# Optimization experiments

Measured on AMD Instinct MI355X. Metric: run time of the kernel, lower is better.

The kernel has to match this reference:

```python
import jax, jax.numpy as jnp
import numpy as np

# Config (matches init_kwargs)
L, B, D, V = 12, 8, 2048, 32000
H, HD, G, N, K = 64, 64, 8, 128, 4
I = H * HD                 # intermediate_size = 4096
CONV = I + 2 * G * N       # conv_dim = 6144
P = I + CONV + H           # in_proj output = 10304
TMAX = 10000.0             # finite replacement for inf time_step_limit


def rmsnorm(x, w, eps=1e-5):
    x32 = x.astype(jnp.float32)
    return (x32 * jax.lax.rsqrt(jnp.mean(x32 * x32, axis=-1, keepdims=True) + eps)) * w


def setup_inputs() -> dict:
    key = jax.random.key(0)
    ks = jax.random.split(key, 10)
    s = 0.02
    return {
        "input_ids": jax.random.randint(ks[0], (B, 1), 0, V),
        "conv_states": jax.random.normal(ks[1], (L, B, CONV, K), dtype=jnp.float32),
        "ssm_states": jax.random.normal(ks[2], (L, B, H, HD, N), dtype=jnp.float32) * 0.1,
        "emb": jax.random.normal(ks[3], (V, D), dtype=jnp.float32) * s,
        "norm_w": jnp.ones((L, D), jnp.float32),
        "in_proj_w": jax.random.normal(ks[4], (L, D, P), dtype=jnp.float32) * s,
        "conv_w": jax.random.normal(ks[5], (L, CONV, K), dtype=jnp.float32) * s,
        "conv_b": jnp.zeros((L, CONV), jnp.float32),
        "dt_bias": jax.random.normal(ks[6], (L, H), dtype=jnp.float32) * s,
        "A_log": jnp.log(jnp.broadcast_to(jnp.arange(1, H + 1, dtype=jnp.float32), (L, H))),
        "D_param": jnp.ones((L, H), jnp.float32),
        "gn_w": jnp.ones((L, I), jnp.float32),
        "out_proj_w": jax.random.normal(ks[7], (L, I, D), dtype=jnp.float32) * s,
        "norm_f_w": jnp.ones((D,), jnp.float32),
        "lm_head_w": jax.random.normal(ks[8], (V, D), dtype=jnp.float32) * s,
    }


def reference(input_ids, conv_states, ssm_states, emb, norm_w, in_proj_w, conv_w,
              conv_b, dt_bias, A_log, D_param, gn_w, out_proj_w, norm_f_w, lm_head_w):
    h = emb[input_ids]  # [B,1,D]

    def layer(h, xs):
        cs, ss, nw, wi, cw, cb, db, al, dp, gw, wo = xs
        residual = h
        hn = rmsnorm(h, nw)                                   # block.norm (RMSNorm)
        proj = jnp.einsum('btd,dp->btp', hn, wi)              # in_proj
        gate, hBC, dt = jnp.split(proj, [I, I + CONV], axis=-1)
        # conv state shift + depthwise conv over kernel dim
        new_in = hBC[:, 0, :]                                 # [B, CONV]
        new_cs = jnp.concatenate([cs[:, :, 1:], new_in[:, :, None]], axis=-1)  # [B,CONV,K]
        conv_out = jnp.sum(new_cs * cw[None], axis=-1) + cb
        conv_out = jax.nn.silu(conv_out)
        x, Bv, Cv = jnp.split(conv_out, [I, I + G * N], axis=-1)
        x = x.reshape(B, H, HD)
        # dt: softplus(dt + dt_bias), clamp to [0, 10000]
        dt_ = jax.nn.softplus(dt[:, 0, :] + db[None, :])       # [B,H]
        dt_ = jnp.clip(dt_, 0.0, TMAX)
        A = -jnp.exp(al)                                       # [H], fp32
        dA = jnp.exp(dt_[:, :, None, None] * A[None, :, None, None])  # [B,H,1,1]
        rep = H // G
        Brep = jnp.repeat(Bv.reshape(B, G, N), rep, axis=1)    # [B,H,N]
        Crep = jnp.repeat(Cv.reshape(B, G, N), rep, axis=1)
        dBx = dt_[:, :, None, None] * Brep[:, :, None, :] * x[:, :, :, None]  # [B,H,HD,N]
        new_ss = ss * dA + dBx
        y = jnp.sum(new_ss * Crep[:, :, None, :], axis=-1)     # [B,H,HD]
        y = y + x * dp[None, :, None]                          # skip via D
        y = y.reshape(B, 1, I)
        # gated RMSNorm: (y * silu(gate)) -> rmsnorm * weight
        yg = y.astype(jnp.float32) * jax.nn.silu(gate.astype(jnp.float32))
        y = rmsnorm(yg, gw)
        out = jnp.einsum('bti,id->btd', y, wo)                 # out_proj
        return residual + out, (new_cs, new_ss)

    h, (new_conv, new_ssm) = jax.lax.scan(
        layer, h,
        (conv_states, ssm_states, norm_w, in_proj_w, conv_w, conv_b,
         dt_bias, A_log, D_param, gn_w, out_proj_w))
    hf = rmsnorm(h, norm_f_w)                                  # norm_f
    logits = jnp.einsum('btd,vd->btv', hf, lm_head_w).astype(jnp.float32)
    return logits, new_conv, new_ssm
```

## Files before the change

kernel.cpp:

```cpp
#include <hip/hip_runtime.h>
#include <hip/hip_bf16.h>
#include <math.h>

#define LNUM 12
#define BNUM 8
#define DNUM 2048
#define VNUM 32000
#define HNUM 64
#define HDNUM 64
#define GNUM 8
#define NNUM 128
#define KNUM 4
#define INUM (HNUM*HDNUM)
#define CONVNUM (INUM + 2*GNUM*NNUM)
#define PNUM (INUM + CONVNUM + HNUM)

#define IP_KC 16
#define OP_KC 64

__device__ __forceinline__ float sigmoidf_(float x){ return 1.f/(1.f+expf(-x)); }

__global__ void k_embed(const int* __restrict__ ids, const float* __restrict__ emb,
                        float* __restrict__ h, float* __restrict__ sqp){
  int b = blockIdx.x; int t = threadIdx.x;
  const float* src = emb + (size_t)ids[b]*DNUM;
  float* dst = h + (size_t)b*DNUM;
  for (int d = t*4; d < DNUM; d += 256*4)
    *(float4*)(dst + d) = *(const float4*)(src + d);
  __shared__ float red[4];
  for (int j = 0; j < 8; ++j){
    float v = src[j*256 + t];
    float q = v*v;
    q += __shfl_xor(q,32); q += __shfl_xor(q,16); q += __shfl_xor(q,8);
    q += __shfl_xor(q,4);  q += __shfl_xor(q,2);  q += __shfl_xor(q,1);
    if ((t & 63) == 0) red[t>>6] = q;
    __syncthreads();
    if (t == 0) sqp[b*8 + j] = red[0]+red[1]+red[2]+red[3];
    __syncthreads();
  }
}

__global__ __launch_bounds__(256) void k_inproj(const float* __restrict__ h,
                                                const float* __restrict__ sqp,
                                                const float* __restrict__ nw,
                                                const float* __restrict__ W,
                                                float* __restrict__ part1){
  int t = threadIdx.x, w = t >> 6, l = t & 63;
  int pb = blockIdx.x, kc = blockIdx.y;
  __shared__ float xs[BNUM][128];
  __shared__ float invs[BNUM];
  __shared__ float4 red[4][BNUM][64];
  if (t < 64){
    int b = t>>3, j = t&7;
    float v = sqp[b*8 + j];
    v += __shfl_xor(v,1); v += __shfl_xor(v,2); v += __shfl_xor(v,4);
    if (j == 0) invs[b] = rsqrtf(v*(1.f/DNUM) + 1e-5f);
  }
  __syncthreads();
  int r0 = kc*128;
  for (int i = t; i < BNUM*128; i += 256){
    int b = i>>7, dl = i&127;
    xs[b][dl] = h[b*DNUM + r0 + dl] * invs[b] * nw[r0 + dl];
  }
  __syncthreads();
  int p0 = pb*256 + l*4;
  bool valid = (p0 < PNUM);
  float4 acc[BNUM];
  #pragma unroll
  for (int b = 0; b < BNUM; ++b) acc[b] = make_float4(0.f,0.f,0.f,0.f);
  if (valid){
    int rbase = w*32;
    const float* wp = W + (size_t)(r0 + rbase)*PNUM + p0;
    #pragma unroll 4
    for (int r = 0; r < 32; ++r){
      float4 w4 = *(const float4*)wp;
      wp += PNUM;
      #pragma unroll
      for (int b = 0; b < BNUM; ++b){
        float xv = xs[b][rbase + r];
        acc[b].x += xv*w4.x; acc[b].y += xv*w4.y; acc[b].z += xv*w4.z; acc[b].w += xv*w4.w;
      }
    }
  }
  #pragma unroll
  for (int b = 0; b < BNUM; ++b) red[w][b][l] = acc[b];
  __syncthreads();
  if (w == 0 && valid){
    #pragma unroll
    for (int b = 0; b < BNUM; ++b){
      float4 s0 = red[0][b][l], s1 = red[1][b][l], s2 = red[2][b][l], s3 = red[3][b][l];
      float4 s;
      s.x = (s0.x+s1.x)+(s2.x+s3.x);
      s.y = (s0.y+s1.y)+(s2.y+s3.y);
      s.z = (s0.z+s1.z)+(s2.z+s3.z);
      s.w = (s0.w+s1.w)+(s2.w+s3.w);
      *(float4*)(part1 + (size_t)(kc*BNUM + b)*PNUM + p0) = s;
    }
  }
}

__global__ void k_convfuse(const float* __restrict__ part1,
                           const float* __restrict__ cs_in, float* __restrict__ cs_out,
                           const float* __restrict__ cw, const float* __restrict__ cb,
                           const float* __restrict__ db, const float* __restrict__ al,
                           float* __restrict__ projg, float* __restrict__ convout,
                           float* __restrict__ dtv, float* __restrict__ dAv){
  int idx = blockIdx.x*256 + threadIdx.x;
  int b = idx / PNUM, p = idx - b*PNUM;
  float v = 0.f;
  #pragma unroll
  for (int kc = 0; kc < IP_KC; ++kc) v += part1[(size_t)(kc*BNUM + b)*PNUM + p];
  if (p < INUM){
    projg[b*INUM + p] = v;
  } else if (p < INUM + CONVNUM){
    int c = p - INUM;
    int sid = b*CONVNUM + c;
    float4 s = *(const float4*)(cs_in + (size_t)sid*KNUM);
    float4 ns = make_float4(s.y, s.z, s.w, v);
    *(float4*)(cs_out + (size_t)sid*KNUM) = ns;
    float4 w = *(const float4*)(cw + c*KNUM);
    float co = ns.x*w.x + ns.y*w.y + ns.z*w.z + ns.w*w.w + cb[c];
    convout[b*CONVNUM + c] = co * sigmoidf_(co);
  } else {
    int hh = p - INUM - CONVNUM;
    float dtr = v + db[hh];
    float dt = (dtr > 20.f) ? dtr : log1pf(expf(dtr));
    dt = fminf(fmaxf(dt, 0.f), 10000.f);
    float A = -expf(al[hh]);
    dtv[b*HNUM + hh] = dt;
    dAv[b*HNUM + hh] = expf(dt*A);
  }
}

__global__ __launch_bounds__(256) void k_ssm(const float* __restrict__ ss_in,
                                             const float* __restrict__ convout,
                                             const float* __restrict__ projg,
                                             const float* __restrict__ dtv,
                                             const float* __restrict__ dAv,
                                             const float* __restrict__ D_param,
                                             float* __restrict__ ss_out,
                                             float* __restrict__ yg,
                                             float* __restrict__ ygsq){
  int b = blockIdx.x >> 6, hh = blockIdx.x & 63;
  int t = threadIdx.x;
  __shared__ float Bs[NNUM], Cs[NNUM];
  __shared__ float sred[8];
  int g = hh >> 3;
  if (t < NNUM) Bs[t] = convout[b*CONVNUM + INUM + g*NNUM + t];
  else          Cs[t-NNUM] = convout[b*CONVNUM + INUM + GNUM*NNUM + g*NNUM + (t-NNUM)];
  __syncthreads();
  float dt = dtv[b*HNUM + hh];
  float dA = dAv[b*HNUM + hh];
  float dp = D_param[hh];
  int r = t & 31, a = t >> 5;
  float4 Bv = *(float4*)&Bs[r*4];
  float4 Cv = *(float4*)&Cs[r*4];
  const float* sin_ = ss_in  + (size_t)(b*HNUM + hh)*HDNUM*NNUM;
  float*       sout = ss_out + (size_t)(b*HNUM + hh)*HDNUM*NNUM;
  float s_yg = 0.f;
  #pragma unroll
  for (int k = 0; k < 8; ++k){
    int hd = k*8 + a;
    float xv = convout[b*CONVNUM + hh*HDNUM + hd];
    float coef = dt * xv;
    int off = k*1024 + t*4;
    float4 s4 = *(const float4*)(sin_ + off);
    float4 ns;
    ns.x = s4.x*dA + coef*Bv.x;
    ns.y = s4.y*dA + coef*Bv.y;
    ns.z = s4.z*dA + coef*Bv.z;
    ns.w = s4.w*dA + coef*Bv.w;
    *(float4*)(sout + off) = ns;
    float yp = ns.x*Cv.x + ns.y*Cv.y + ns.z*Cv.z + ns.w*Cv.w;
    yp += __shfl_xor(yp,1); yp += __shfl_xor(yp,2); yp += __shfl_xor(yp,4);
    yp += __shfl_xor(yp,8); yp += __shfl_xor(yp,16);
    if (r == 0){
      float gv = projg[b*INUM + hh*HDNUM + hd];
      float ygv = (yp + xv*dp) * gv * sigmoidf_(gv);
      yg[b*INUM + hh*HDNUM + hd] = ygv;
      s_yg += ygv*ygv;
    }
  }
  if (r == 0) sred[a] = s_yg;
  __syncthreads();
  if (t == 0){
    float tot = 0.f;
    #pragma unroll
    for (int j = 0; j < 8; ++j) tot += sred[j];
    ygsq[b*HNUM + hh] = tot;
  }
}

__global__ __launch_bounds__(256) void k_outproj(const float* __restrict__ yg,
                                                 const float* __restrict__ ygsq,
                                                 const float* __restrict__ gw,
                                                 const float* __restrict__ W,
                                                 float* __restrict__ part2){
  int t = threadIdx.x, w = t >> 6, l = t & 63;
  int pb = blockIdx.x, kc = blockIdx.y;
  __shared__ float xs[BNUM][64];
  __shared__ float invg[BNUM];
  __shared__ float4 red[4][BNUM][64];
  if (t < 64){
    int b = t>>3, j = t&7;
    float v = 0.f;
    #pragma unroll
    for (int jj = 0; jj < 8; ++jj) v += ygsq[b*HNUM + j + jj*8];
    v += __shfl_xor(v,1); v += __shfl_xor(v,2); v += __shfl_xor(v,4);
    if (j == 0) invg[b] = rsqrtf(v*(1.f/INUM) + 1e-5f);
  }
  __syncthreads();
  int r0 = kc*64;
  for (int i = t; i < BNUM*64; i += 256){
    int b = i>>6, il = i&63;
    xs[b][il] = yg[b*INUM + r0 + il] * invg[b] * gw[r0 + il];
  }
  __syncthreads();
  int d0 = pb*256 + l*4;
  float4 acc[BNUM];
  #pragma unroll
  for (int b = 0; b < BNUM; ++b) acc[b] = make_float4(0.f,0.f,0.f,0.f);
  {
    int rbase = w*16;
    const float* wp = W + (size_t)(r0 + rbase)*DNUM + d0;
    #pragma unroll 4
    for (int r = 0; r < 16; ++r){
      float4 w4 = *(const float4*)wp;
      wp += DNUM;
      #pragma unroll
      for (int b = 0; b < BNUM; ++b){
        float xv = xs[b][rbase + r];
        acc[b].x += xv*w4.x; acc[b].y += xv*w4.y; acc[b].z += xv*w4.z; acc[b].w += xv*w4.w;
      }
    }
  }
  #pragma unroll
  for (int b = 0; b < BNUM; ++b) red[w][b][l] = acc[b];
  __syncthreads();
  if (w == 0){
    #pragma unroll
    for (int b = 0; b < BNUM; ++b){
      float4 s0 = red[0][b][l], s1 = red[1][b][l], s2 = red[2][b][l], s3 = red[3][b][l];
      float4 s;
      s.x = (s0.x+s1.x)+(s2.x+s3.x);
      s.y = (s0.y+s1.y)+(s2.y+s3.y);
      s.z = (s0.z+s1.z)+(s2.z+s3.z);
      s.w = (s0.w+s1.w)+(s2.w+s3.w);
      *(float4*)(part2 + (size_t)(kc*BNUM + b)*DNUM + d0) = s;
    }
  }
}

__global__ void k_reduce_out(const float* __restrict__ part2, float* __restrict__ h,
                             float* __restrict__ sqp){
  int idx = blockIdx.x*256 + threadIdx.x;
  float s = h[idx];
  #pragma unroll
  for (int ic = 0; ic < OP_KC; ++ic) s += part2[(size_t)ic*BNUM*DNUM + idx];
  h[idx] = s;
  float q = s*s;
  q += __shfl_xor(q,32); q += __shfl_xor(q,16); q += __shfl_xor(q,8);
  q += __shfl_xor(q,4);  q += __shfl_xor(q,2);  q += __shfl_xor(q,1);
  __shared__ float red[4];
  int t = threadIdx.x;
  if ((t & 63) == 0) red[t>>6] = q;
  __syncthreads();
  if (t == 0) sqp[blockIdx.x] = red[0]+red[1]+red[2]+red[3];
}

__global__ __launch_bounds__(256) void k_lmhead(const float* __restrict__ h,
                                                const float* __restrict__ sqp,
                                                const float* __restrict__ nf,
                                                const float* __restrict__ Wl,
                                                float* __restrict__ logits){
  __shared__ float hs[BNUM*DNUM];
  int t = threadIdx.x;
  float invb[8];
  #pragma unroll
  for (int b2 = 0; b2 < 8; ++b2){
    float s = 0.f;
    #pragma unroll
    for (int j = 0; j < 8; ++j) s += sqp[b2*8 + j];
    invb[b2] = rsqrtf(s*(1.f/DNUM) + 1e-5f);
  }
  #pragma unroll
  for (int it = 0; it < 16; ++it){
    int i = t*4 + it*1024;
    float iv = invb[it>>1];
    float4 hv  = *(const float4*)(h + i);
    float4 nfv = *(const float4*)(nf + (i & 2047));
    float4 o;
    o.x = hv.x*iv*nfv.x; o.y = hv.y*iv*nfv.y; o.z = hv.z*iv*nfv.z; o.w = hv.w*iv*nfv.w;
    *(float4*)(hs + i) = o;
  }
  __syncthreads();
  int wv = t >> 6, lane = t & 63;
  int v0 = (blockIdx.x*4 + wv)*4;
  float acc[4][BNUM];
  #pragma unroll
  for (int u = 0; u < 4; ++u)
    #pragma unroll
    for (int b = 0; b < BNUM; ++b) acc[u][b] = 0.f;
  #pragma unroll
  for (int j = 0; j < 8; ++j){
    int dbase = j*256 + lane*4;
    float4 w0 = *(const float4*)(Wl + (size_t)(v0+0)*DNUM + dbase);
    float4 w1 = *(const float4*)(Wl + (size_t)(v0+1)*DNUM + dbase);
    float4 w2 = *(const float4*)(Wl + (size_t)(v0+2)*DNUM + dbase);
    float4 w3 = *(const float4*)(Wl + (size_t)(v0+3)*DNUM + dbase);
    #pragma unroll
    for (int b = 0; b < BNUM; ++b){
      float4 hv = *(const float4*)(hs + b*DNUM + dbase);
      acc[0][b] += w0.x*hv.x + w0.y*hv.y + w0.z*hv.z + w0.w*hv.w;
      acc[1][b] += w1.x*hv.x + w1.y*hv.y + w1.z*hv.z + w1.w*hv.w;
      acc[2][b] += w2.x*hv.x + w2.y*hv.y + w2.z*hv.z + w2.w*hv.w;
      acc[3][b] += w3.x*hv.x + w3.y*hv.y + w3.z*hv.z + w3.w*hv.w;
    }
  }
  #pragma unroll
  for (int u = 0; u < 4; ++u)
    #pragma unroll
    for (int b = 0; b < BNUM; ++b){
      float s = acc[u][b];
      s += __shfl_xor(s,32); s += __shfl_xor(s,16); s += __shfl_xor(s,8);
      s += __shfl_xor(s,4);  s += __shfl_xor(s,2);  s += __shfl_xor(s,1);
      if (lane == 0) logits[(size_t)b*VNUM + v0 + u] = s;
    }
}

extern "C" void kernel_launch(void* const* d_in, const int* in_sizes, int n_in,
                              void* d_out, int out_size, void* d_ws, size_t ws_size,
                              hipStream_t stream){
  const int*   ids         = (const int*)d_in[0];
  const float* conv_states = (const float*)d_in[1];
  const float* ssm_states  = (const float*)d_in[2];
  const float* emb         = (const float*)d_in[3];
  const float* norm_w      = (const float*)d_in[4];
  const float* in_proj_w   = (const float*)d_in[5];
  const float* conv_w      = (const float*)d_in[6];
  const float* conv_b      = (const float*)d_in[7];
  const float* dt_bias     = (const float*)d_in[8];
  const float* A_log       = (const float*)d_in[9];
  const float* D_param     = (const float*)d_in[10];
  const float* gn_w        = (const float*)d_in[11];
  const float* out_proj_w  = (const float*)d_in[12];
  const float* norm_f_w    = (const float*)d_in[13];
  const float* lm_head_w   = (const float*)d_in[14];

  float* out         = (float*)d_out;
  float* logits      = out;
  float* conv_out_st = out + (size_t)BNUM*VNUM;
  float* ssm_out_st  = conv_out_st + (size_t)LNUM*BNUM*CONVNUM*KNUM;

  float* ws      = (float*)d_ws;
  float* h       = ws;
  float* projg   = h      + 16384;
  float* convout = projg  + 32768;
  float* dtv     = convout+ 49152;
  float* dAv     = dtv    + 512;
  float* yg      = dAv    + 512;
  float* ygsq    = yg     + 32768;
  float* sqp     = ygsq   + 512;
  float* part1   = sqp    + 64;
  float* part2   = part1  + 1830912;

  k_embed<<<BNUM, 256, 0, stream>>>(ids, emb, h, sqp);

  for (int l = 0; l < LNUM; ++l){
    dim3 g1(56, IP_KC);
    k_inproj<<<g1, 256, 0, stream>>>(h, sqp, norm_w + (size_t)l*DNUM,
                                     in_proj_w + (size_t)l*DNUM*PNUM, part1);
    k_convfuse<<<(BNUM*PNUM)/256, 256, 0, stream>>>(
        part1,
        conv_states + (size_t)l*BNUM*CONVNUM*KNUM,
        conv_out_st + (size_t)l*BNUM*CONVNUM*KNUM,
        conv_w + (size_t)l*CONVNUM*KNUM, conv_b + (size_t)l*CONVNUM,
        dt_bias + (size_t)l*HNUM, A_log + (size_t)l*HNUM,
        projg, convout, dtv, dAv);
    k_ssm<<<BNUM*HNUM, 256, 0, stream>>>(
        ssm_states + (size_t)l*BNUM*HNUM*HDNUM*NNUM, convout, projg, dtv, dAv,
        D_param + (size_t)l*HNUM,
        ssm_out_st + (size_t)l*BNUM*HNUM*HDNUM*NNUM, yg, ygsq);
    dim3 g2(8, OP_KC);
    k_outproj<<<g2, 256, 0, stream>>>(yg, ygsq, gn_w + (size_t)l*INUM,
                                      out_proj_w + (size_t)l*INUM*DNUM, part2);
    k_reduce_out<<<64, 256, 0, stream>>>(part2, h, sqp);
  }

  k_lmhead<<<VNUM/16, 256, 0, stream>>>(h, sqp, norm_f_w, lm_head_w, logits);
}
```

Baseline: 946.1 us.

## Fuse all layer kernels into one persistent kernel with grid-wide barriers

Replaces the 61 per-layer kernel launches (in_proj, conv, ssm, out_proj, reduce) with a single persistent 512-block kernel that uses atomic-counter grid barriers between phases. The conv and dt work is folded into the SSM phase, with each block recomputing its own conv channels from the partial sums, so projg/convout/dtv/dAv buffers are no longer needed. This removes launch gaps and some intermediate global traffic. In exchange it relies on all 512 blocks being co-resident, has a spin-wait barrier with a timeout escape, and runs in_proj with fewer resident blocks than before.

New measurement: 3.470 ms. +266.8%, slower.

```diff
diff --git a/kernel.cpp b/kernel.cpp
--- a/kernel.cpp
+++ b/kernel.cpp
@@ -17,255 +17,319 @@
 
 #define IP_KC 16
 #define OP_KC 64
+#define GRID 512
+
+struct MParams {
+  const int* ids;
+  const float* conv_states; const float* ssm_states;
+  const float* emb; const float* norm_w; const float* in_proj_w;
+  const float* conv_w; const float* conv_b; const float* dt_bias;
+  const float* A_log; const float* D_param; const float* gn_w;
+  const float* out_proj_w;
+  float* conv_out_st; float* ssm_out_st;
+  float* h; float* yg; float* ygsq; float* sqp; float* part1; float* part2;
+  int* bar_cnt;
+};
 
 __device__ __forceinline__ float sigmoidf_(float x){ return 1.f/(1.f+expf(-x)); }
 
-__global__ void k_embed(const int* __restrict__ ids, const float* __restrict__ emb,
-                        float* __restrict__ h, float* __restrict__ sqp){
-  int b = blockIdx.x; int t = threadIdx.x;
-  const float* src = emb + (size_t)ids[b]*DNUM;
-  float* dst = h + (size_t)b*DNUM;
-  for (int d = t*4; d < DNUM; d += 256*4)
-    *(float4*)(dst + d) = *(const float4*)(src + d);
-  __shared__ float red[4];
-  for (int j = 0; j < 8; ++j){
-    float v = src[j*256 + t];
-    float q = v*v;
-    q += __shfl_xor(q,32); q += __shfl_xor(q,16); q += __shfl_xor(q,8);
-    q += __shfl_xor(q,4);  q += __shfl_xor(q,2);  q += __shfl_xor(q,1);
-    if ((t & 63) == 0) red[t>>6] = q;
-    __syncthreads();
-    if (t == 0) sqp[b*8 + j] = red[0]+red[1]+red[2]+red[3];
-    __syncthreads();
-  }
+__device__ __forceinline__ void gbar(int* cnt, int target){
+  __syncthreads();
+  if (threadIdx.x == 0){
+    __threadfence();
+    __hip_atomic_fetch_add(cnt, 1, __ATOMIC_RELAXED, __HIP_MEMORY_SCOPE_AGENT);
+    long spins = 0;
+    while (__hip_atomic_load(cnt, __ATOMIC_RELAXED, __HIP_MEMORY_SCOPE_AGENT) < target){
+      __builtin_amdgcn_s_sleep(2);
+      if (++spins > (1L<<22)) break;
+    }
+    __threadfence();
+  }
+  __syncthreads();
 }
 
-__global__ __launch_bounds__(256) void k_inproj(const float* __restrict__ h,
-                                                const float* __restrict__ sqp,
-                                                const float* __restrict__ nw,
-                                                const float* __restrict__ W,
-                                                float* __restrict__ part1){
-  int t = threadIdx.x, w = t >> 6, l = t & 63;
-  int pb = blockIdx.x, kc = blockIdx.y;
-  __shared__ float xs[BNUM][128];
-  __shared__ float invs[BNUM];
-  __shared__ float4 red[4][BNUM][64];
-  if (t < 64){
-    int b = t>>3, j = t&7;
-    float v = sqp[b*8 + j];
-    v += __shfl_xor(v,1); v += __shfl_xor(v,2); v += __shfl_xor(v,4);
-    if (j == 0) invs[b] = rsqrtf(v*(1.f/DNUM) + 1e-5f);
-  }
-  __syncthreads();
-  int r0 = kc*128;
-  for (int i = t; i < BNUM*128; i += 256){
-    int b = i>>7, dl = i&127;
-    xs[b][dl] = h[b*DNUM + r0 + dl] * invs[b] * nw[r0 + dl];
-  }
-  __syncthreads();
-  int p0 = pb*256 + l*4;
-  bool valid = (p0 < PNUM);
-  float4 acc[BNUM];
-  #pragma unroll
-  for (int b = 0; b < BNUM; ++b) acc[b] = make_float4(0.f,0.f,0.f,0.f);
-  if (valid){
-    int rbase = w*32;
-    const float* wp = W + (size_t)(r0 + rbase)*PNUM + p0;
-    #pragma unroll 4
-    for (int r = 0; r < 32; ++r){
-      float4 w4 = *(const float4*)wp;
-      wp += PNUM;
-      #pragma unroll
-      for (int b = 0; b < BNUM; ++b){
-        float xv = xs[b][rbase + r];
-        acc[b].x += xv*w4.x; acc[b].y += xv*w4.y; acc[b].z += xv*w4.z; acc[b].w += xv*w4.w;
+__global__ __launch_bounds__(256, 2) void k_mamba(MParams P){
+  const int blk = blockIdx.x, t = threadIdx.x;
+  const int w = t >> 6, l = t & 63;
+  __shared__ float smem[3088];
+  int bar_no = 0;
+
+  if (blk < BNUM){
+    int b = blk;
+    const float* src = P.emb + (size_t)P.ids[b]*DNUM;
+    float* dst = P.h + (size_t)b*DNUM;
+    float4 v0 = *(const float4*)(src + t*4);
+    float4 v1 = *(const float4*)(src + 1024 + t*4);
+    *(float4*)(dst + t*4) = v0;
+    *(float4*)(dst + 1024 + t*4) = v1;
+    float q0 = v0.x*v0.x+v0.y*v0.y+v0.z*v0.z+v0.w*v0.w;
+    float q1 = v1.x*v1.x+v1.y*v1.y+v1.z*v1.z+v1.w*v1.w;
+    q0 += __shfl_xor(q0,1); q0 += __shfl_xor(q0,2); q0 += __shfl_xor(q0,4); q0 += __shfl_xor(q0,8);
+    q1 += __shfl_xor(q1,1); q1 += __shfl_xor(q1,2); q1 += __shfl_xor(q1,4); q1 += __shfl_xor(q1,8);
+    if ((t & 15) == 0){
+      P.sqp[b*32 + (t>>4)]      = q0;
+      P.sqp[b*32 + 16 + (t>>4)] = q1;
+    }
+  }
+  gbar(P.bar_cnt, GRID * (++bar_no));
+
+  for (int li = 0; li < LNUM; ++li){
+    const float* Wi   = P.in_proj_w  + (size_t)li*DNUM*PNUM;
+    const float* nw   = P.norm_w     + (size_t)li*DNUM;
+    const float* cw   = P.conv_w     + (size_t)li*CONVNUM*KNUM;
+    const float* cb   = P.conv_b     + (size_t)li*CONVNUM;
+    const float* db   = P.dt_bias    + (size_t)li*HNUM;
+    const float* al   = P.A_log      + (size_t)li*HNUM;
+    const float* dpp  = P.D_param    + (size_t)li*HNUM;
+    const float* gw   = P.gn_w       + (size_t)li*INUM;
+    const float* Wo   = P.out_proj_w + (size_t)li*INUM*DNUM;
+    const float* csin = P.conv_states + (size_t)li*BNUM*CONVNUM*KNUM;
+    float*       csout= P.conv_out_st + (size_t)li*BNUM*CONVNUM*KNUM;
+    const float* ssin = P.ssm_states  + (size_t)li*BNUM*HNUM*HDNUM*NNUM;
+    float*       ssout= P.ssm_out_st  + (size_t)li*BNUM*HNUM*HDNUM*NNUM;
+
+    {
+      float* xs   = smem;
+      float* invs = smem + 1024;
+      float4* red = (float4*)(smem + 1040);
+      for (int vb = blk; vb < 896; vb += GRID){
+        int pb = vb % 56, kc = vb / 56;
+        if (t < 64){
+          int b = t>>3, j = t&7;
+          float v = P.sqp[b*32+j] + P.sqp[b*32+8+j] + P.sqp[b*32+16+j] + P.sqp[b*32+24+j];
+          v += __shfl_xor(v,1); v += __shfl_xor(v,2); v += __shfl_xor(v,4);
+          if (j == 0) invs[b] = rsqrtf(v*(1.f/DNUM) + 1e-5f);
+        }
+        __syncthreads();
+        int r0 = kc*128;
+        for (int i = t; i < BNUM*128; i += 256){
+          int b = i>>7, dl = i&127;
+          xs[i] = P.h[b*DNUM + r0 + dl] * invs[b] * nw[r0 + dl];
+        }
+        __syncthreads();
+        int p0 = pb*256 + l*4;
+        bool valid = (p0 < PNUM);
+        float4 acc[BNUM];
+        #pragma unroll
+        for (int b = 0; b < BNUM; ++b) acc[b] = make_float4(0.f,0.f,0.f,0.f);
+        if (valid){
+          int rbase = w*32;
+          const float* wp = Wi + (size_t)(r0 + rbase)*PNUM + p0;
+          #pragma unroll 4
+          for (int r = 0; r < 32; ++r){
+            float4 w4 = *(const float4*)wp;
+            wp += PNUM;
+            #pragma unroll
+            for (int b = 0; b < BNUM; ++b){
+              float xvv = xs[b*128 + rbase + r];
+              acc[b].x += xvv*w4.x; acc[b].y += xvv*w4.y; acc[b].z += xvv*w4.z; acc[b].w += xvv*w4.w;
+            }
+          }
+        }
+        #pragma unroll
+        for (int rw = 1; rw < 4; ++rw){
+          if (w == rw){
+            #pragma unroll
+            for (int b = 0; b < BNUM; ++b) red[b*64 + l] = acc[b];
+          }
+          __syncthreads();
+          if (w == 0){
+            #pragma unroll
+            for (int b = 0; b < BNUM; ++b){
+              float4 r4 = red[b*64 + l];
+              acc[b].x += r4.x; acc[b].y += r4.y; acc[b].z += r4.z; acc[b].w += r4.w;
+            }
+          }
+          __syncthreads();
+        }
+        if (w == 0 && valid){
+          #pragma unroll
+          for (int b = 0; b < BNUM; ++b)
+            *(float4*)(P.part1 + (size_t)(kc*BNUM + b)*PNUM + p0) = acc[b];
+        }
+        __syncthreads();
       }
     }
-  }
-  #pragma unroll
-  for (int b = 0; b < BNUM; ++b) red[w][b][l] = acc[b];
-  __syncthreads();
-  if (w == 0 && valid){
-    #pragma unroll
-    for (int b = 0; b < BNUM; ++b){
-      float4 s0 = red[0][b][l], s1 = red[1][b][l], s2 = red[2][b][l], s3 = red[3][b][l];
-      float4 s;
-      s.x = (s0.x+s1.x)+(s2.x+s3.x);
-      s.y = (s0.y+s1.y)+(s2.y+s3.y);
-      s.z = (s0.z+s1.z)+(s2.z+s3.z);
-      s.w = (s0.w+s1.w)+(s2.w+s3.w);
-      *(float4*)(part1 + (size_t)(kc*BNUM + b)*PNUM + p0) = s;
-    }
-  }
-}
-
-__global__ void k_convfuse(const float* __restrict__ part1,
-                           const float* __restrict__ cs_in, float* __restrict__ cs_out,
-                           const float* __restrict__ cw, const float* __restrict__ cb,
-                           const float* __restrict__ db, const float* __restrict__ al,
-                           float* __restrict__ projg, float* __restrict__ convout,
-                           float* __restrict__ dtv, float* __restrict__ dAv){
-  int idx = blockIdx.x*256 + threadIdx.x;
-  int b = idx / PNUM, p = idx - b*PNUM;
-  float v = 0.f;
-  #pragma unroll
-  for (int kc = 0; kc < IP_KC; ++kc) v += part1[(size_t)(kc*BNUM + b)*PNUM + p];
-  if (p < INUM){
-    projg[b*INUM + p] = v;
-  } else if (p < INUM + CONVNUM){
-    int c = p - INUM;
-    int sid = b*CONVNUM + c;
-    float4 s = *(const float4*)(cs_in + (size_t)sid*KNUM);
-    float4 ns = make_float4(s.y, s.z, s.w, v);
-    *(float4*)(cs_out + (size_t)sid*KNUM) = ns;
-    float4 w = *(const float4*)(cw + c*KNUM);
-    float co = ns.x*w.x + ns.y*w.y + ns.z*w.z + ns.w*w.w + cb[c];
-    convout[b*CONVNUM + c] = co * sigmoidf_(co);
-  } else {
-    int hh = p - INUM - CONVNUM;
-    float dtr = v + db[hh];
-    float dt = (dtr > 20.f) ? dtr : log1pf(expf(dtr));
-    dt = fminf(fmaxf(dt, 0.f), 10000.f);
-    float A = -expf(al[hh]);
-    dtv[b*HNUM + hh] = dt;
-    dAv[b*HNUM + hh] = expf(dt*A);
-  }
-}
-
-__global__ __launch_bounds__(256) void k_ssm(const float* __restrict__ ss_in,
-                                             const float* __restrict__ convout,
-                                             const float* __restrict__ projg,
-                                             const float* __restrict__ dtv,
-                                             const float* __restrict__ dAv,
-                                             const float* __restrict__ D_param,
-                                             float* __restrict__ ss_out,
-                                             float* __restrict__ yg,
-                                             float* __restrict__ ygsq){
-  int b = blockIdx.x >> 6, hh = blockIdx.x & 63;
-  int t = threadIdx.x;
-  __shared__ float Bs[NNUM], Cs[NNUM];
-  __shared__ float sred[8];
-  int g = hh >> 3;
-  if (t < NNUM) Bs[t] = convout[b*CONVNUM + INUM + g*NNUM + t];
-  else          Cs[t-NNUM] = convout[b*CONVNUM + INUM + GNUM*NNUM + g*NNUM + (t-NNUM)];
-  __syncthreads();
-  float dt = dtv[b*HNUM + hh];
-  float dA = dAv[b*HNUM + hh];
-  float dp = D_param[hh];
-  int r = t & 31, a = t >> 5;
-  float4 Bv = *(float4*)&Bs[r*4];
-  float4 Cv = *(float4*)&Cs[r*4];
-  const float* sin_ = ss_in  + (size_t)(b*HNUM + hh)*HDNUM*NNUM;
-  float*       sout = ss_out + (size_t)(b*HNUM + hh)*HDNUM*NNUM;
-  float s_yg = 0.f;
-  #pragma unroll
-  for (int k = 0; k < 8; ++k){
-    int hd = k*8 + a;
-    float xv = convout[b*CONVNUM + hh*HDNUM + hd];
-    float coef = dt * xv;
-    int off = k*1024 + t*4;
-    float4 s4 = *(const float4*)(sin_ + off);
-    float4 ns;
-    ns.x = s4.x*dA + coef*Bv.x;
-    ns.y = s4.y*dA + coef*Bv.y;
-    ns.z = s4.z*dA + coef*Bv.z;
-    ns.w = s4.w*dA + coef*Bv.w;
-    *(float4*)(sout + off) = ns;
-    float yp = ns.x*Cv.x + ns.y*Cv.y + ns.z*Cv.z + ns.w*Cv.w;
-    yp += __shfl_xor(yp,1); yp += __shfl_xor(yp,2); yp += __shfl_xor(yp,4);
-    yp += __shfl_xor(yp,8); yp += __shfl_xor(yp,16);
-    if (r == 0){
-      float gv = projg[b*INUM + hh*HDNUM + hd];
-      float ygv = (yp + xv*dp) * gv * sigmoidf_(gv);
-      yg[b*INUM + hh*HDNUM + hd] = ygv;
-      s_yg += ygv*ygv;
-    }
-  }
-  if (r == 0) sred[a] = s_yg;
-  __syncthreads();
-  if (t == 0){
-    float tot = 0.f;
-    #pragma unroll
-    for (int j = 0; j < 8; ++j) tot += sred[j];
-    ygsq[b*HNUM + hh] = tot;
-  }
-}
-
-__global__ __launch_bounds__(256) void k_outproj(const float* __restrict__ yg,
-                                                 const float* __restrict__ ygsq,
-                                                 const float* __restrict__ gw,
-                                                 const float* __restrict__ W,
-                                                 float* __restrict__ part2){
-  int t = threadIdx.x, w = t >> 6, l = t & 63;
-  int pb = blockIdx.x, kc = blockIdx.y;
-  __shared__ float xs[BNUM][64];
-  __shared__ float invg[BNUM];
-  __shared__ float4 red[4][BNUM][64];
-  if (t < 64){
-    int b = t>>3, j = t&7;
-    float v = 0.f;
-    #pragma unroll
-    for (int jj = 0; jj < 8; ++jj) v += ygsq[b*HNUM + j + jj*8];
-    v += __shfl_xor(v,1); v += __shfl_xor(v,2); v += __shfl_xor(v,4);
-    if (j == 0) invg[b] = rsqrtf(v*(1.f/INUM) + 1e-5f);
-  }
-  __syncthreads();
-  int r0 = kc*64;
-  for (int i = t; i < BNUM*64; i += 256){
-    int b = i>>6, il = i&63;
-    xs[b][il] = yg[b*INUM + r0 + il] * invg[b] * gw[r0 + il];
-  }
-  __syncthreads();
-  int d0 = pb*256 + l*4;
-  float4 acc[BNUM];
-  #pragma unroll
-  for (int b = 0; b < BNUM; ++b) acc[b] = make_float4(0.f,0.f,0.f,0.f);
-  {
-    int rbase = w*16;
-    const float* wp = W + (size_t)(r0 + rbase)*DNUM + d0;
-    #pragma unroll 4
-    for (int r = 0; r < 16; ++r){
-      float4 w4 = *(const float4*)wp;
-      wp += DNUM;
-      #pragma unroll
-      for (int b = 0; b < BNUM; ++b){
-        float xv = xs[b][rbase + r];
-        acc[b].x += xv*w4.x; acc[b].y += xv*w4.y; acc[b].z += xv*w4.z; acc[b].w += xv*w4.w;
+    gbar(P.bar_cnt, GRID * (++bar_no));
+
+    {
+      float* xv    = smem;
+      float* Bsh   = smem + 64;
+      float* Csh   = smem + 192;
+      float* gatel = smem + 320;
+      float* scal  = smem + 384;
+      float* sred  = smem + 392;
+      {
+        int b = blk >> 6, hh = blk & 63, g = hh >> 3;
+        {
+          int c, kind, n;
+          if (t < 64)      { kind=0; n=t;     c = hh*HDNUM + t; }
+          else if (t < 192){ kind=1; n=t-64;  c = INUM + g*NNUM + n; }
+          else             { kind=2; n=t-192; c = INUM + GNUM*NNUM + g*NNUM + n; }
+          int p = INUM + c;
+          float v = 0.f;
+          #pragma unroll
+          for (int kc2 = 0; kc2 < IP_KC; ++kc2) v += P.part1[(size_t)(kc2*BNUM + b)*PNUM + p];
+          size_t sid = (size_t)b*CONVNUM + c;
+          float4 s4 = *(const float4*)(csin + sid*KNUM);
+          float4 ns = make_float4(s4.y, s4.z, s4.w, v);
+          if (kind == 0 || (hh & 7) == 0) *(float4*)(csout + sid*KNUM) = ns;
+          float4 w4 = *(const float4*)(cw + (size_t)c*KNUM);
+          float co = ns.x*w4.x + ns.y*w4.y + ns.z*w4.z + ns.w*w4.w + cb[c];
+          float sv = co * sigmoidf_(co);
+          if (kind == 0) xv[n] = sv; else if (kind == 1) Bsh[n] = sv; else Csh[n] = sv;
+        }
+        if (t < 64){
+          int n = 64 + t; int c = INUM + GNUM*NNUM + g*NNUM + n; int p = INUM + c;
+          float v = 0.f;
+          #pragma unroll
+          for (int kc2 = 0; kc2 < IP_KC; ++kc2) v += P.part1[(size_t)(kc2*BNUM + b)*PNUM + p];
+          size_t sid = (size_t)b*CONVNUM + c;
+          float4 s4 = *(const float4*)(csin + sid*KNUM);
+          float4 ns = make_float4(s4.y, s4.z, s4.w, v);
+          if ((hh & 7) == 0) *(float4*)(csout + sid*KNUM) = ns;
+          float4 w4 = *(const float4*)(cw + (size_t)c*KNUM);
+          float co = ns.x*w4.x + ns.y*w4.y + ns.z*w4.z + ns.w*w4.w + cb[c];
+          Csh[n] = co * sigmoidf_(co);
+        } else if (t < 128){
+          int gc = hh*HDNUM + (t-64);
+          float v = 0.f;
+          #pragma unroll
+          for (int kc2 = 0; kc2 < IP_KC; ++kc2) v += P.part1[(size_t)(kc2*BNUM + b)*PNUM + gc];
+          gatel[t-64] = v;
+        } else if (t == 128){
+          int p = INUM + CONVNUM + hh;
+          float v = 0.f;
+          #pragma unroll
+          for (int kc2 = 0; kc2 < IP_KC; ++kc2) v += P.part1[(size_t)(kc2*BNUM + b)*PNUM + p];
+          float dtr = v + db[hh];
+          float dt = (dtr > 20.f) ? dtr : log1pf(expf(dtr));
+          dt = fminf(dt, 10000.f);
+          scal[0] = dt;
+          scal[1] = expf(dt * (-expf(al[hh])));
+        }
+        __syncthreads();
+        float dt = scal[0], dA = scal[1], dp = dpp[hh];
+        int r = t & 31, a2 = t >> 5;
+        float4 Bv = *(float4*)&Bsh[r*4];
+        float4 Cv = *(float4*)&Csh[r*4];
+        const float* si = ssin  + (size_t)(b*HNUM + hh)*HDNUM*NNUM;
+        float*       so = ssout + (size_t)(b*HNUM + hh)*HDNUM*NNUM;
+        float s_yg = 0.f;
+        #pragma unroll
+        for (int k = 0; k < 8; ++k){
+          int hd = k*8 + a2;
+          float xvv = xv[hd];
+          float coef = dt * xvv;
+          int off = k*1024 + t*4;
+          float4 s4 = *(const float4*)(si + off);
+          float4 ns;
+          ns.x = s4.x*dA + coef*Bv.x;
+          ns.y = s4.y*dA + coef*Bv.y;
+          ns.z = s4.z*dA + coef*Bv.z;
+          ns.w = s4.w*dA + coef*Bv.w;
+          *(float4*)(so + off) = ns;
+          float yp = ns.x*Cv.x + ns.y*Cv.y + ns.z*Cv.z + ns.w*Cv.w;
+          yp += __shfl_xor(yp,1); yp += __shfl_xor(yp,2); yp += __shfl_xor(yp,4);
+          yp += __shfl_xor(yp,8); yp += __shfl_xor(yp,16);
+          if (r == 0){
+            float gv = gatel[hd];
+            float ygv = (yp + xvv*dp) * gv * sigmoidf_(gv);
+            P.yg[b*INUM + hh*HDNUM + hd] = ygv;
+            s_yg += ygv*ygv;
+          }
+        }
+        if (r == 0) sred[a2] = s_yg;
+        __syncthreads();
+        if (t == 0){
+          float tot = 0.f;
+          #pragma unroll
+          for (int j = 0; j < 8; ++j) tot += sred[j];
+          P.ygsq[b*HNUM + hh] = tot;
+        }
       }
     }
-  }
-  #pragma unroll
-  for (int b = 0; b < BNUM; ++b) red[w][b][l] = acc[b];
-  __syncthreads();
-  if (w == 0){
-    #pragma unroll
-    for (int b = 0; b < BNUM; ++b){
-      float4 s0 = red[0][b][l], s1 = red[1][b][l], s2 = red[2][b][l], s3 = red[3][b][l];
-      float4 s;
-      s.x = (s0.x+s1.x)+(s2.x+s3.x);
-      s.y = (s0.y+s1.y)+(s2.y+s3.y);
-      s.z = (s0.z+s1.z)+(s2.z+s3.z);
-      s.w = (s0.w+s1.w)+(s2.w+s3.w);
-      *(float4*)(part2 + (size_t)(kc*BNUM + b)*DNUM + d0) = s;
-    }
-  }
-}
-
-__global__ void k_reduce_out(const float* __restrict__ part2, float* __restrict__ h,
-                             float* __restrict__ sqp){
-  int idx = blockIdx.x*256 + threadIdx.x;
-  float s = h[idx];
-  #pragma unroll
-  for (int ic = 0; ic < OP_KC; ++ic) s += part2[(size_t)ic*BNUM*DNUM + idx];
-  h[idx] = s;
-  float q = s*s;
-  q += __shfl_xor(q,32); q += __shfl_xor(q,16); q += __shfl_xor(q,8);
-  q += __shfl_xor(q,4);  q += __shfl_xor(q,2);  q += __shfl_xor(q,1);
-  __shared__ float red[4];
-  int t = threadIdx.x;
-  if ((t & 63) == 0) red[t>>6] = q;
-  __syncthreads();
-  if (t == 0) sqp[blockIdx.x] = red[0]+red[1]+red[2]+red[3];
+    gbar(P.bar_cnt, GRID * (++bar_no));
+
+    {
+      float* xs   = smem;
+      float* invg = smem + 512;
+      float4* red = (float4*)(smem + 520);
+      {
+        int pb = blk & 7, kc = blk >> 3;
+        if (t < 64){
+          int b = t>>3, j = t&7;
+          float v = 0.f;
+          #pragma unroll
+          for (int jj = 0; jj < 8; ++jj) v += P.ygsq[b*HNUM + j + jj*8];
+          v += __shfl_xor(v,1); v += __shfl_xor(v,2); v += __shfl_xor(v,4);
+          if (j == 0) invg[b] = rsqrtf(v*(1.f/INUM) + 1e-5f);
+        }
+        __syncthreads();
+        int r0 = kc*64;
+        for (int i = t; i < BNUM*64; i += 256){
+          int b = i>>6, il = i&63;
+          xs[i] = P.yg[b*INUM + r0 + il] * invg[b] * gw[r0 + il];
+        }
+        __syncthreads();
+        int d0 = pb*256 + l*4;
+        float4 acc[BNUM];
+        #pragma unroll
+        for (int b = 0; b < BNUM; ++b) acc[b] = make_float4(0.f,0.f,0.f,0.f);
+        {
+          int rbase = w*16;
+          const float* wp = Wo + (size_t)(r0 + rbase)*DNUM + d0;
+          #pragma unroll 4
+          for (int r2 = 0; r2 < 16; ++r2){
+            float4 w4 = *(const float4*)wp;
+            wp += DNUM;
+            #pragma unroll
+            for (int b = 0; b < BNUM; ++b){
+              float xvv = xs[b*64 + rbase + r2];
+              acc[b].x += xvv*w4.x; acc[b].y += xvv*w4.y; acc[b].z += xvv*w4.z; acc[b].w += xvv*w4.w;
+            }
+          }
+        }
+        #pragma unroll
+        for (int rw = 1; rw < 4; ++rw){
+          if (w == rw){
+            #pragma unroll
+            for (int b = 0; b < BNUM; ++b) red[b*64 + l] = acc[b];
+          }
+          __syncthreads();
+          if (w == 0){
+            #pragma unroll
+            for (int b = 0; b < BNUM; ++b){
+              float4 r4 = red[b*64 + l];
+              acc[b].x += r4.x; acc[b].y += r4.y; acc[b].z += r4.z; acc[b].w += r4.w;
+            }
+          }
+          __syncthreads();
+        }
+        if (w == 0){
+          #pragma unroll
+          for (int b = 0; b < BNUM; ++b)
+            *(float4*)(P.part2 + (size_t)(kc*BNUM + b)*DNUM + d0) = acc[b];
+        }
+      }
+    }
+    gbar(P.bar_cnt, GRID * (++bar_no));
+
+    {
+      if (blk < 64){
+        int idx = blk*256 + t;
+        float s = P.h[idx];
+        #pragma unroll 8
+        for (int ic = 0; ic < OP_KC; ++ic) s += P.part2[(size_t)ic*BNUM*DNUM + idx];
+        P.h[idx] = s;
+        float q = s*s;
+        q += __shfl_xor(q,32); q += __shfl_xor(q,16); q += __shfl_xor(q,8);
+        q += __shfl_xor(q,4);  q += __shfl_xor(q,2);  q += __shfl_xor(q,1);
+        if (l == 0) P.sqp[idx>>6] = q;
+      }
+    }
+    gbar(P.bar_cnt, GRID * (++bar_no));
+  }
 }
 
 __global__ __launch_bounds__(256) void k_lmhead(const float* __restrict__ h,
@@ -274,19 +338,19 @@
                                                 const float* __restrict__ Wl,
                                                 float* __restrict__ logits){
   __shared__ float hs[BNUM*DNUM];
+  __shared__ float invb_s[8];
   int t = threadIdx.x;
-  float invb[8];
-  #pragma unroll
-  for (int b2 = 0; b2 < 8; ++b2){
+  if (t < 8){
     float s = 0.f;
     #pragma unroll
-    for (int j = 0; j < 8; ++j) s += sqp[b2*8 + j];
-    invb[b2] = rsqrtf(s*(1.f/DNUM) + 1e-5f);
-  }
+    for (int j = 0; j < 32; ++j) s += sqp[t*32 + j];
+    invb_s[t] = rsqrtf(s*(1.f/DNUM) + 1e-5f);
+  }
+  __syncthreads();
   #pragma unroll
   for (int it = 0; it < 16; ++it){
     int i = t*4 + it*1024;
-    float iv = invb[it>>1];
+    float iv = invb_s[it>>1];
     float4 hv  = *(const float4*)(h + i);
     float4 nfv = *(const float4*)(nf + (i & 2047));
     float4 o;
@@ -352,40 +416,27 @@
   float* conv_out_st = out + (size_t)BNUM*VNUM;
   float* ssm_out_st  = conv_out_st + (size_t)LNUM*BNUM*CONVNUM*KNUM;
 
-  float* ws      = (float*)d_ws;
-  float* h       = ws;
-  float* projg   = h      + 16384;
-  float* convout = projg  + 32768;
-  float* dtv     = convout+ 49152;
-  float* dAv     = dtv    + 512;
-  float* yg      = dAv    + 512;
-  float* ygsq    = yg     + 32768;
-  float* sqp     = ygsq   + 512;
-  float* part1   = sqp    + 64;
-  float* part2   = part1  + 1830912;
-
-  k_embed<<<BNUM, 256, 0, stream>>>(ids, emb, h, sqp);
-
-  for (int l = 0; l < LNUM; ++l){
-    dim3 g1(56, IP_KC);
-    k_inproj<<<g1, 256, 0, stream>>>(h, sqp, norm_w + (size_t)l*DNUM,
-                                     in_proj_w + (size_t)l*DNUM*PNUM, part1);
-    k_convfuse<<<(BNUM*PNUM)/256, 256, 0, stream>>>(
-        part1,
-        conv_states + (size_t)l*BNUM*CONVNUM*KNUM,
-        conv_out_st + (size_t)l*BNUM*CONVNUM*KNUM,
-        conv_w + (size_t)l*CONVNUM*KNUM, conv_b + (size_t)l*CONVNUM,
-        dt_bias + (size_t)l*HNUM, A_log + (size_t)l*HNUM,
-        projg, convout, dtv, dAv);
-    k_ssm<<<BNUM*HNUM, 256, 0, stream>>>(
-        ssm_states + (size_t)l*BNUM*HNUM*HDNUM*NNUM, convout, projg, dtv, dAv,
-        D_param + (size_t)l*HNUM,
-        ssm_out_st + (size_t)l*BNUM*HNUM*HDNUM*NNUM, yg, ygsq);
-    dim3 g2(8, OP_KC);
-    k_outproj<<<g2, 256, 0, stream>>>(yg, ygsq, gn_w + (size_t)l*INUM,
-                                      out_proj_w + (size_t)l*INUM*DNUM, part2);
-    k_reduce_out<<<64, 256, 0, stream>>>(part2, h, sqp);
-  }
-
+  float* ws    = (float*)d_ws;
+  float* h     = ws;
+  float* yg    = h    + 16384;
+  float* ygsq  = yg   + 32768;
+  float* sqp   = ygsq + 512;
+  float* part1 = sqp  + 256;
+  float* part2 = part1+ 1830912;
+  int*   bar   = (int*)(part2 + 1048576);
+
+  hipMemsetAsync(bar, 0, 128, stream);
+
+  MParams P;
+  P.ids = ids; P.conv_states = conv_states; P.ssm_states = ssm_states;
+  P.emb = emb; P.norm_w = norm_w; P.in_proj_w = in_proj_w;
+  P.conv_w = conv_w; P.conv_b = conv_b; P.dt_bias = dt_bias;
+  P.A_log = A_log; P.D_param = D_param; P.gn_w = gn_w;
+  P.out_proj_w = out_proj_w;
+  P.conv_out_st = conv_out_st; P.ssm_out_st = ssm_out_st;
+  P.h = h; P.yg = yg; P.ygsq = ygsq; P.sqp = sqp; P.part1 = part1; P.part2 = part2;
+  P.bar_cnt = bar;
+
+  k_mamba<<<GRID, 256, 0, stream>>>(P);
   k_lmhead<<<VNUM/16, 256, 0, stream>>>(h, sqp, norm_f_w, lm_head_w, logits);
 }
```
